# Optimization experiments

Measured on AMD Instinct MI355X. Metric: run time of the kernel, lower is better.

Reference implementation:

```python
import jax, jax.numpy as jnp
import numpy as np

N_QUBITS = 4
N_LAYERS = 2
_I2 = jnp.eye(2, dtype=jnp.complex64)
_X = jnp.array([[0.0, 1.0], [1.0, 0.0]], dtype=jnp.complex64)


def _apply_1q_batched(state, U, wire):
    # state: [B,2,2,2,2] complex, U: [B,2,2] (per-sample gate)
    s = jnp.moveaxis(state, 1 + wire, -1)
    s = jnp.einsum('bij,b...j->b...i', U, s)
    return jnp.moveaxis(s, -1, 1 + wire)


def _apply_1q(state, U, wire):
    # shared 2x2 gate on `wire`
    s = jnp.moveaxis(state, 1 + wire, -1)
    s = jnp.einsum('ij,...j->...i', U, s)
    return jnp.moveaxis(s, -1, 1 + wire)


def _apply_cnot(state, c, t):
    s = jnp.moveaxis(state, (1 + c, 1 + t), (-2, -1))  # [...,2(ctrl),2(tgt)]
    s = jnp.stack([s[..., 0, :], s[..., 1, ::-1]], axis=-2)  # flip target if ctrl=1
    return jnp.moveaxis(s, (-2, -1), (1 + c, 1 + t))


def _rot_matrix(phi, theta, omega):
    # qml.Rot = RZ(omega) @ RY(theta) @ RZ(phi)
    c, s = jnp.cos(theta / 2), jnp.sin(theta / 2)
    ep = jnp.exp(-0.5j * (phi + omega))  # e^{-i(phi+omega)/2}
    em = jnp.exp(-0.5j * (phi - omega))  # e^{-i(phi-omega)/2}
    return jnp.stack([
        jnp.stack([ep * c, -jnp.conj(em) * s]),
        jnp.stack([em * s, jnp.conj(ep) * c]),
    ]).astype(jnp.complex64)


def _circuit(angles, weights):
    # angles: [B, 4] real; weights: [2, 4, 3] real -> [B, 4] PauliZ expvals
    B = angles.shape[0]
    state = jnp.zeros((B,) + (2,) * N_QUBITS, jnp.complex64)
    state = state.at[(slice(None),) + (0,) * N_QUBITS].set(1.0)  # |0000>
    # AngleEmbedding (rotation='X'): RX(angle_w) on wire w, batched over samples
    for w in range(N_QUBITS):
        half = angles[:, w] / 2
        c, s = jnp.cos(half), jnp.sin(half)
        U = c[:, None, None] * _I2 - 1j * s[:, None, None] * _X  # [B,2,2]
        state = _apply_1q_batched(state, U, w)
    # StronglyEntanglingLayers: Rot on each wire, then ring of CNOTs with range r
    for l in range(N_LAYERS):
        for w in range(N_QUBITS):
            U = _rot_matrix(weights[l, w, 0], weights[l, w, 1], weights[l, w, 2])
            state = _apply_1q(state, U, w)
        r = (l % (N_QUBITS - 1)) + 1  # PennyLane default ranges
        for w in range(N_QUBITS):
            state = _apply_cnot(state, w, (w + r) % N_QUBITS)
    probs = state.real ** 2 + state.imag ** 2  # [B,2,2,2,2]
    z = []
    for w in range(N_QUBITS):
        other = tuple(a for a in range(1, N_QUBITS + 1) if a != 1 + w)
        p = probs.sum(other)  # [B,2]
        z.append(p[:, 0] - p[:, 1])
    return jnp.stack(z, axis=-1)  # [B,4]


def setup_inputs() -> dict:
    key = jax.random.key(0)
    ks = jax.random.split(key, 6)
    B, D_IN, D_OUT, NQ = 65536, 512, 512, N_QUBITS
    x = jax.random.normal(ks[0], (B, D_IN), jnp.float32)
    pre_W = jax.random.normal(ks[1], (NQ, D_IN), jnp.float32) / np.sqrt(D_IN)
    pre_b = jax.random.normal(ks[2], (NQ,), jnp.float32) * 0.05
    weights = jax.random.uniform(ks[3], (N_LAYERS, NQ, 3), jnp.float32) * (2 * np.pi)
    post_W = jax.random.normal(ks[4], (D_OUT, NQ), jnp.float32) / np.sqrt(NQ)
    post_b = jax.random.normal(ks[5], (D_OUT,), jnp.float32) * 0.05
    return {"x": x, "pre_W": pre_W, "pre_b": pre_b, "weights": weights,
            "post_W": post_W, "post_b": post_b}


def reference(x, pre_W, pre_b, weights, post_W, post_b):
    angles = jnp.tanh(x @ pre_W.T + pre_b) * jnp.pi  # [B,4]
    q = _circuit(angles, weights)                    # [B,4]
    return q @ post_W.T + post_b                     # [B,512]
```

## Files before the change

kernel.cpp:

```cpp
#include <hip/hip_runtime.h>
#include <math.h>

#define PI_F 3.14159265358979323846f


typedef float floatx4 __attribute__((ext_vector_type(4)));

static __device__ __forceinline__ void st_store4(float* p, floatx4 v)
{
    *reinterpret_cast<floatx4*>(p) = v;
}

static __device__ __forceinline__ float fast_tanh(float a)
{
    a = fminf(fmaxf(a, -15.f), 15.f);
    const float e = __expf(2.f * a);
    return (e - 1.f) / (e + 1.f);
}

template<int WIRE>
__device__ __forceinline__ void apply1q(float* sr, float* si,
    float u00r, float u00i, float u01r, float u01i,
    float u10r, float u10i, float u11r, float u11i)
{
    constexpr int st = 1 << (3 - WIRE);
#pragma unroll
    for (int i = 0; i < 16; ++i) {
        if (i & st) continue;
        const int j = i | st;
        const float r0 = sr[i], m0 = si[i], r1 = sr[j], m1 = si[j];
        sr[i] = u00r * r0 - u00i * m0 + u01r * r1 - u01i * m1;
        si[i] = u00r * m0 + u00i * r0 + u01r * m1 + u01i * r1;
        sr[j] = u10r * r0 - u10i * m0 + u11r * r1 - u11i * m1;
        si[j] = u10r * m0 + u10i * r0 + u11r * m1 + u11i * r1;
    }
}

template<int CW, int TW>
__device__ __forceinline__ void cnot(float* sr, float* si)
{
    constexpr int cb = 1 << (3 - CW), tb = 1 << (3 - TW);
#pragma unroll
    for (int i = 0; i < 16; ++i) {
        if ((i & cb) && !(i & tb)) {
            const int j = i | tb;
            float t;
            t = sr[i]; sr[i] = sr[j]; sr[j] = t;
            t = si[i]; si[i] = si[j]; si[j] = t;
        }
    }
}

#define APPLY_FAST(L, W) { \
    const float ph = wts[((L) * 4 + (W)) * 3 + 0]; \
    const float th = wts[((L) * 4 + (W)) * 3 + 1]; \
    const float om = wts[((L) * 4 + (W)) * 3 + 2]; \
    const float s_  = __sinf(0.5f * th),        c_  = __cosf(0.5f * th); \
    const float sp_ = __sinf(0.5f * (ph + om)), cp_ = __cosf(0.5f * (ph + om)); \
    const float sq_ = __sinf(0.5f * (ph - om)), cq_ = __cosf(0.5f * (ph - om)); \
    apply1q<W>(sr, si, cp_ * c_, -sp_ * c_, -cq_ * s_, -sq_ * s_, \
                       cq_ * s_, -sq_ * s_, cp_ * c_,  sp_ * c_); }

__global__ __launch_bounds__(256) void k_fused(
    const float* __restrict__ x,
    const float* __restrict__ preW,
    const float* __restrict__ preb,
    const float* __restrict__ wts,
    const float* __restrict__ postW,
    const float* __restrict__ postb,
    float* __restrict__ out, int B)
{
    const int lane  = threadIdx.x & 63;
    const int wid   = threadIdx.x >> 6;
    const int base  = blockIdx.x * 64;
    const int wbase = base + wid * 16;
    if (base >= B) return;

    __shared__ float4 angLds[64];

    float4 wA[4], wB[4];
#pragma unroll
    for (int w = 0; w < 4; ++w) {
        wA[w] = *reinterpret_cast<const float4*>(preW + w * 512 + lane * 4);
        wB[w] = *reinterpret_cast<const float4*>(preW + w * 512 + 256 + lane * 4);
    }
    const float4 pb = *reinterpret_cast<const float4*>(preb);

#pragma unroll
    for (int p = 0; p < 4; ++p) {
        const int b0 = wbase + p * 4;

        float4 xa[4], xb[4];
#pragma unroll
        for (int t = 0; t < 4; ++t) {
            const float* xr = x + (size_t)(b0 + t) * 512;
            xa[t] = *reinterpret_cast<const float4*>(xr + lane * 4);
            xb[t] = *reinterpret_cast<const float4*>(xr + 256 + lane * 4);
        }

        float acc[4][4];
#pragma unroll
        for (int t = 0; t < 4; ++t) {
#pragma unroll
            for (int w = 0; w < 4; ++w) {
                acc[t][w] = xa[t].x * wA[w].x + xa[t].y * wA[w].y + xa[t].z * wA[w].z + xa[t].w * wA[w].w
                          + xb[t].x * wB[w].x + xb[t].y * wB[w].y + xb[t].z * wB[w].z + xb[t].w * wB[w].w;
            }
        }

        float v[4];
#pragma unroll
        for (int t = 0; t < 4; ++t) {
            float a01 = (lane & 1) ? acc[t][1] : acc[t][0];
            float b01 = (lane & 1) ? acc[t][0] : acc[t][1];
            a01 += __shfl_xor(b01, 1, 64);
            float a23 = (lane & 1) ? acc[t][3] : acc[t][2];
            float b23 = (lane & 1) ? acc[t][2] : acc[t][3];
            a23 += __shfl_xor(b23, 1, 64);
            const float vv = (lane & 2) ? a23 : a01;
            const float uu = (lane & 2) ? a01 : a23;
            v[t] = vv + __shfl_xor(uu, 2, 64);
        }
        float c01 = (lane & 4) ? v[1] : v[0];
        float d01 = (lane & 4) ? v[0] : v[1];
        c01 += __shfl_xor(d01, 4, 64);
        float c23 = (lane & 4) ? v[3] : v[2];
        float d23 = (lane & 4) ? v[2] : v[3];
        c23 += __shfl_xor(d23, 4, 64);
        float m = (lane & 8) ? c23 : c01;
        float n = (lane & 8) ? c01 : c23;
        m += __shfl_xor(n, 8, 64);
        m += __shfl_xor(m, 16, 64);
        m += __shfl_xor(m, 32, 64);

        const float pb01 = (lane & 1) ? pb.y : pb.x;
        const float pb23 = (lane & 1) ? pb.w : pb.z;
        const float pbv  = (lane & 2) ? pb23 : pb01;
        const float angv = fast_tanh(m + pbv) * PI_F;

        if (lane < 16) {
            float* arow = reinterpret_cast<float*>(&angLds[wid * 16 + p * 4 + (lane >> 2)]);
            arow[lane & 3] = angv;
        }
    }

    __syncthreads();

    const int sid = lane >> 2;
    const float4 ang = angLds[wid * 16 + sid];

    const float s0 = __sinf(0.5f * ang.x), c0 = __cosf(0.5f * ang.x);
    const float s1 = __sinf(0.5f * ang.y), c1 = __cosf(0.5f * ang.y);
    const float s2 = __sinf(0.5f * ang.z), c2 = __cosf(0.5f * ang.z);
    const float s3 = __sinf(0.5f * ang.w), c3 = __cosf(0.5f * ang.w);

    float sr[16], si[16];
#pragma unroll
    for (int i = 0; i < 16; ++i) {
        const float r = ((i & 8) ? s0 : c0) * ((i & 4) ? s1 : c1)
                      * ((i & 2) ? s2 : c2) * ((i & 1) ? s3 : c3);
        const int mm = (((i >> 3) & 1) + ((i >> 2) & 1) + ((i >> 1) & 1) + (i & 1)) & 3;
        switch (mm) {
            case 0:  sr[i] = r;    si[i] = 0.f; break;
            case 1:  sr[i] = 0.f;  si[i] = -r;  break;
            case 2:  sr[i] = -r;   si[i] = 0.f; break;
            default: sr[i] = 0.f;  si[i] = r;   break;
        }
    }

    APPLY_FAST(0, 0); APPLY_FAST(0, 1); APPLY_FAST(0, 2); APPLY_FAST(0, 3);
    cnot<0, 1>(sr, si); cnot<1, 2>(sr, si); cnot<2, 3>(sr, si); cnot<3, 0>(sr, si);
    APPLY_FAST(1, 0); APPLY_FAST(1, 1); APPLY_FAST(1, 2); APPLY_FAST(1, 3);
    cnot<0, 2>(sr, si); cnot<1, 3>(sr, si); cnot<2, 0>(sr, si); cnot<3, 1>(sr, si);

    float z0 = 0.f, z1 = 0.f, z2 = 0.f, z3 = 0.f;
#pragma unroll
    for (int i = 0; i < 16; ++i) {
        const float p = sr[i] * sr[i] + si[i] * si[i];
        z0 += (i & 8) ? -p : p;
        z1 += (i & 4) ? -p : p;
        z2 += (i & 2) ? -p : p;
        z3 += (i & 1) ? -p : p;
    }

    const float4* pW4 = reinterpret_cast<const float4*>(postW);
    const float4* pb4 = reinterpret_cast<const float4*>(postb);
    const float4 p0 = pW4[4 * lane + 0], p1 = pW4[4 * lane + 1];
    const float4 p2 = pW4[4 * lane + 2], p3 = pW4[4 * lane + 3];
    const float4 p4 = pW4[4 * (64 + lane) + 0], p5 = pW4[4 * (64 + lane) + 1];
    const float4 p6 = pW4[4 * (64 + lane) + 2], p7 = pW4[4 * (64 + lane) + 3];
    const float4 bb0 = pb4[lane], bb1 = pb4[64 + lane];

#pragma unroll
    for (int s = 0; s < 16; ++s) {
        const float q0 = __shfl(z0, s * 4, 64);
        const float q1 = __shfl(z1, s * 4, 64);
        const float q2 = __shfl(z2, s * 4, 64);
        const float q3 = __shfl(z3, s * 4, 64);
        floatx4 o0, o1;
        o0.x = fmaf(q3, p0.w, fmaf(q2, p0.z, fmaf(q1, p0.y, fmaf(q0, p0.x, bb0.x))));
        o0.y = fmaf(q3, p1.w, fmaf(q2, p1.z, fmaf(q1, p1.y, fmaf(q0, p1.x, bb0.y))));
        o0.z = fmaf(q3, p2.w, fmaf(q2, p2.z, fmaf(q1, p2.y, fmaf(q0, p2.x, bb0.z))));
        o0.w = fmaf(q3, p3.w, fmaf(q2, p3.z, fmaf(q1, p3.y, fmaf(q0, p3.x, bb0.w))));
        o1.x = fmaf(q3, p4.w, fmaf(q2, p4.z, fmaf(q1, p4.y, fmaf(q0, p4.x, bb1.x))));
        o1.y = fmaf(q3, p5.w, fmaf(q2, p5.z, fmaf(q1, p5.y, fmaf(q0, p5.x, bb1.y))));
        o1.z = fmaf(q3, p6.w, fmaf(q2, p6.z, fmaf(q1, p6.y, fmaf(q0, p6.x, bb1.z))));
        o1.w = fmaf(q3, p7.w, fmaf(q2, p7.z, fmaf(q1, p7.y, fmaf(q0, p7.x, bb1.w))));
        float* orow = out + (size_t)(wbase + s) * 512;
        st_store4(orow + 4 * lane, o0);
        st_store4(orow + 256 + 4 * lane, o1);
    }
}

extern "C" void kernel_launch(void* const* d_in, const int* in_sizes, int n_in,
                              void* d_out, int out_size, void* d_ws, size_t ws_size,
                              hipStream_t stream)
{
    const float* x     = (const float*)d_in[0];
    const float* preW  = (const float*)d_in[1];
    const float* preb  = (const float*)d_in[2];
    const float* wts   = (const float*)d_in[3];
    const float* postW = (const float*)d_in[4];
    const float* postb = (const float*)d_in[5];
    float* out = (float*)d_out;
    const int B = in_sizes[0] / 512;

    k_fused<<<dim3((B + 63) / 64), dim3(256), 0, stream>>>(
        x, preW, preb, wts, postW, postb, out, B);
}
```

Baseline: 50.34 us.

## Distribute 16-amplitude state vector across 4 lanes with shuffle-based gates

Result: faster. 46.13 us (-8.4%).

```diff
diff --git a/kernel.cpp b/kernel.cpp
--- a/kernel.cpp
+++ b/kernel.cpp
@@ -18,48 +18,51 @@
     return (e - 1.f) / (e + 1.f);
 }
 
-template<int WIRE>
-__device__ __forceinline__ void apply1q(float* sr, float* si,
+template<int ST>
+__device__ __forceinline__ void rot_inlane(float* ar, float* ai,
     float u00r, float u00i, float u01r, float u01i,
     float u10r, float u10i, float u11r, float u11i)
 {
-    constexpr int st = 1 << (3 - WIRE);
-#pragma unroll
-    for (int i = 0; i < 16; ++i) {
-        if (i & st) continue;
-        const int j = i | st;
-        const float r0 = sr[i], m0 = si[i], r1 = sr[j], m1 = si[j];
-        sr[i] = u00r * r0 - u00i * m0 + u01r * r1 - u01i * m1;
-        si[i] = u00r * m0 + u00i * r0 + u01r * m1 + u01i * r1;
-        sr[j] = u10r * r0 - u10i * m0 + u11r * r1 - u11i * m1;
-        si[j] = u10r * m0 + u10i * r0 + u11r * m1 + u11i * r1;
-    }
-}
-
-template<int CW, int TW>
-__device__ __forceinline__ void cnot(float* sr, float* si)
-{
-    constexpr int cb = 1 << (3 - CW), tb = 1 << (3 - TW);
-#pragma unroll
-    for (int i = 0; i < 16; ++i) {
-        if ((i & cb) && !(i & tb)) {
-            const int j = i | tb;
-            float t;
-            t = sr[i]; sr[i] = sr[j]; sr[j] = t;
-            t = si[i]; si[i] = si[j]; si[j] = t;
-        }
-    }
-}
-
-#define APPLY_FAST(L, W) { \
-    const float ph = wts[((L) * 4 + (W)) * 3 + 0]; \
-    const float th = wts[((L) * 4 + (W)) * 3 + 1]; \
-    const float om = wts[((L) * 4 + (W)) * 3 + 2]; \
-    const float s_  = __sinf(0.5f * th),        c_  = __cosf(0.5f * th); \
-    const float sp_ = __sinf(0.5f * (ph + om)), cp_ = __cosf(0.5f * (ph + om)); \
-    const float sq_ = __sinf(0.5f * (ph - om)), cq_ = __cosf(0.5f * (ph - om)); \
-    apply1q<W>(sr, si, cp_ * c_, -sp_ * c_, -cq_ * s_, -sq_ * s_, \
-                       cq_ * s_, -sq_ * s_, cp_ * c_,  sp_ * c_); }
+#pragma unroll
+    for (int k = 0; k < 4; ++k) {
+        if (k & ST) continue;
+        const int j = k | ST;
+        const float Ar = ar[k], Ai = ai[k], Br = ar[j], Bi = ai[j];
+        ar[k] = u00r*Ar - u00i*Ai + u01r*Br - u01i*Bi;
+        ai[k] = u00r*Ai + u00i*Ar + u01r*Bi + u01i*Br;
+        ar[j] = u10r*Ar - u10i*Ai + u11r*Br - u11i*Bi;
+        ai[j] = u10r*Ai + u10i*Ar + u11r*Bi + u11i*Br;
+    }
+}
+
+template<int XM>
+__device__ __forceinline__ void rot_cross(float* ar, float* ai, bool ownB,
+    float u00r, float u00i, float u01r, float u01i,
+    float u10r, float u10i, float u11r, float u11i)
+{
+    const float cAr = ownB ? u11r : u00r;
+    const float cAi = ownB ? u11i : u00i;
+    const float cBr = ownB ? u10r : u01r;
+    const float cBi = ownB ? u10i : u01i;
+#pragma unroll
+    for (int k = 0; k < 4; ++k) {
+        const float pr = __shfl_xor(ar[k], XM, 64);
+        const float pi = __shfl_xor(ai[k], XM, 64);
+        const float vr = ar[k], vi = ai[k];
+        ar[k] = cAr*vr - cAi*vi + cBr*pr - cBi*pi;
+        ai[k] = cAr*vi + cAi*vr + cBr*pi + cBi*pr;
+    }
+}
+
+#define ROT_COEFFS(L, W) \
+    const float ph = wts[((L)*4+(W))*3+0]; \
+    const float th = wts[((L)*4+(W))*3+1]; \
+    const float om = wts[((L)*4+(W))*3+2]; \
+    const float s_  = __sinf(0.5f*th),        c_  = __cosf(0.5f*th); \
+    const float sp_ = __sinf(0.5f*(ph+om)),   cp_ = __cosf(0.5f*(ph+om)); \
+    const float sq_ = __sinf(0.5f*(ph-om)),   cq_ = __cosf(0.5f*(ph-om));
+
+#define U_ARGS cp_*c_, -sp_*c_, -cq_*s_, -sq_*s_, cq_*s_, -sq_*s_, cp_*c_, sp_*c_
 
 __global__ __launch_bounds__(256) void k_fused(
     const float* __restrict__ x,
@@ -146,7 +149,9 @@
 
     __syncthreads();
 
-    const int sid = lane >> 2;
+    const int  sid = lane >> 2;
+    const bool lb3 = (lane & 2) != 0;
+    const bool lb2 = (lane & 1) != 0;
     const float4 ang = angLds[wid * 16 + sid];
 
     const float s0 = __sinf(0.5f * ang.x), c0 = __cosf(0.5f * ang.x);
@@ -154,41 +159,97 @@
     const float s2 = __sinf(0.5f * ang.z), c2 = __cosf(0.5f * ang.z);
     const float s3 = __sinf(0.5f * ang.w), c3 = __cosf(0.5f * ang.w);
 
-    float sr[16], si[16];
-#pragma unroll
-    for (int i = 0; i < 16; ++i) {
-        const float r = ((i & 8) ? s0 : c0) * ((i & 4) ? s1 : c1)
-                      * ((i & 2) ? s2 : c2) * ((i & 1) ? s3 : c3);
-        const int mm = (((i >> 3) & 1) + ((i >> 2) & 1) + ((i >> 1) & 1) + (i & 1)) & 3;
-        switch (mm) {
-            case 0:  sr[i] = r;    si[i] = 0.f; break;
-            case 1:  sr[i] = 0.f;  si[i] = -r;  break;
-            case 2:  sr[i] = -r;   si[i] = 0.f; break;
-            default: sr[i] = 0.f;  si[i] = r;   break;
-        }
-    }
-
-    APPLY_FAST(0, 0); APPLY_FAST(0, 1); APPLY_FAST(0, 2); APPLY_FAST(0, 3);
-    cnot<0, 1>(sr, si); cnot<1, 2>(sr, si); cnot<2, 3>(sr, si); cnot<3, 0>(sr, si);
-    APPLY_FAST(1, 0); APPLY_FAST(1, 1); APPLY_FAST(1, 2); APPLY_FAST(1, 3);
-    cnot<0, 2>(sr, si); cnot<1, 3>(sr, si); cnot<2, 0>(sr, si); cnot<3, 1>(sr, si);
-
-    float z0 = 0.f, z1 = 0.f, z2 = 0.f, z3 = 0.f;
-#pragma unroll
-    for (int i = 0; i < 16; ++i) {
-        const float p = sr[i] * sr[i] + si[i] * si[i];
-        z0 += (i & 8) ? -p : p;
-        z1 += (i & 4) ? -p : p;
-        z2 += (i & 2) ? -p : p;
-        z3 += (i & 1) ? -p : p;
-    }
+    const float mhi = (lb3 ? s0 : c0) * (lb2 ? s1 : c1);
+    const float hr  = lb3 ? (lb2 ? -mhi : 0.f) : (lb2 ? 0.f : mhi);
+    const float hi  = (lb3 != lb2) ? -mhi : 0.f;
+    const float low0 = c2 * c3, low1 = c2 * s3, low2 = s2 * c3, low3 = s2 * s3;
+
+    float ar[4], ai[4];
+    ar[0] =  hr * low0;  ai[0] =  hi * low0;
+    ar[1] =  hi * low1;  ai[1] = -hr * low1;
+    ar[2] =  hi * low2;  ai[2] = -hr * low2;
+    ar[3] = -hr * low3;  ai[3] = -hi * low3;
+
+    { ROT_COEFFS(0, 0); rot_cross<2>(ar, ai, lb3, U_ARGS); }
+    { ROT_COEFFS(0, 1); rot_cross<1>(ar, ai, lb2, U_ARGS); }
+    { ROT_COEFFS(0, 2); rot_inlane<2>(ar, ai, U_ARGS); }
+    { ROT_COEFFS(0, 3); rot_inlane<1>(ar, ai, U_ARGS); }
+
+    {
+#pragma unroll
+        for (int k = 0; k < 4; ++k) {
+            const float tr = __shfl_xor(ar[k], 1, 64);
+            const float ti = __shfl_xor(ai[k], 1, 64);
+            ar[k] = lb3 ? tr : ar[k];
+            ai[k] = lb3 ? ti : ai[k];
+        }
+    }
+    {
+        const float t0r = ar[0], t0i = ai[0], t1r = ar[1], t1i = ai[1];
+        ar[0] = lb2 ? ar[2] : ar[0];  ai[0] = lb2 ? ai[2] : ai[0];
+        ar[1] = lb2 ? ar[3] : ar[1];  ai[1] = lb2 ? ai[3] : ai[1];
+        ar[2] = lb2 ? t0r   : ar[2];  ai[2] = lb2 ? t0i   : ai[2];
+        ar[3] = lb2 ? t1r   : ar[3];  ai[3] = lb2 ? t1i   : ai[3];
+    }
+    {
+        float t;
+        t = ar[2]; ar[2] = ar[3]; ar[3] = t;
+        t = ai[2]; ai[2] = ai[3]; ai[3] = t;
+    }
+    {
+        ar[1] = __shfl_xor(ar[1], 2, 64);  ai[1] = __shfl_xor(ai[1], 2, 64);
+        ar[3] = __shfl_xor(ar[3], 2, 64);  ai[3] = __shfl_xor(ai[3], 2, 64);
+    }
+
+    { ROT_COEFFS(1, 0); rot_cross<2>(ar, ai, lb3, U_ARGS); }
+    { ROT_COEFFS(1, 1); rot_cross<1>(ar, ai, lb2, U_ARGS); }
+    { ROT_COEFFS(1, 2); rot_inlane<2>(ar, ai, U_ARGS); }
+    { ROT_COEFFS(1, 3); rot_inlane<1>(ar, ai, U_ARGS); }
+
+    {
+        const float t0r = ar[0], t0i = ai[0], t1r = ar[1], t1i = ai[1];
+        ar[0] = lb3 ? ar[2] : ar[0];  ai[0] = lb3 ? ai[2] : ai[0];
+        ar[1] = lb3 ? ar[3] : ar[1];  ai[1] = lb3 ? ai[3] : ai[1];
+        ar[2] = lb3 ? t0r   : ar[2];  ai[2] = lb3 ? t0i   : ai[2];
+        ar[3] = lb3 ? t1r   : ar[3];  ai[3] = lb3 ? t1i   : ai[3];
+    }
+    {
+        const float t0r = ar[0], t0i = ai[0], t2r = ar[2], t2i = ai[2];
+        ar[0] = lb2 ? ar[1] : ar[0];  ai[0] = lb2 ? ai[1] : ai[0];
+        ar[1] = lb2 ? t0r   : ar[1];  ai[1] = lb2 ? t0i   : ai[1];
+        ar[2] = lb2 ? ar[3] : ar[2];  ai[2] = lb2 ? ai[3] : ai[2];
+        ar[3] = lb2 ? t2r   : ar[3];  ai[3] = lb2 ? t2i   : ai[3];
+    }
+    {
+        ar[2] = __shfl_xor(ar[2], 2, 64);  ai[2] = __shfl_xor(ai[2], 2, 64);
+        ar[3] = __shfl_xor(ar[3], 2, 64);  ai[3] = __shfl_xor(ai[3], 2, 64);
+    }
+    {
+        ar[1] = __shfl_xor(ar[1], 1, 64);  ai[1] = __shfl_xor(ai[1], 1, 64);
+        ar[3] = __shfl_xor(ar[3], 1, 64);  ai[3] = __shfl_xor(ai[3], 1, 64);
+    }
+
+    const float p0 = ar[0]*ar[0] + ai[0]*ai[0];
+    const float p1 = ar[1]*ar[1] + ai[1]*ai[1];
+    const float p2 = ar[2]*ar[2] + ai[2]*ai[2];
+    const float p3 = ar[3]*ar[3] + ai[3]*ai[3];
+    const float s01 = p0 + p1, s23 = p2 + p3;
+    const float sum = s01 + s23;
+    float z0 = lb3 ? -sum : sum;
+    float z1 = lb2 ? -sum : sum;
+    float z2 = s01 - s23;
+    float z3 = (p0 - p1) + (p2 - p3);
+    z0 += __shfl_xor(z0, 1, 64);  z0 += __shfl_xor(z0, 2, 64);
+    z1 += __shfl_xor(z1, 1, 64);  z1 += __shfl_xor(z1, 2, 64);
+    z2 += __shfl_xor(z2, 1, 64);  z2 += __shfl_xor(z2, 2, 64);
+    z3 += __shfl_xor(z3, 1, 64);  z3 += __shfl_xor(z3, 2, 64);
 
     const float4* pW4 = reinterpret_cast<const float4*>(postW);
     const float4* pb4 = reinterpret_cast<const float4*>(postb);
-    const float4 p0 = pW4[4 * lane + 0], p1 = pW4[4 * lane + 1];
-    const float4 p2 = pW4[4 * lane + 2], p3 = pW4[4 * lane + 3];
-    const float4 p4 = pW4[4 * (64 + lane) + 0], p5 = pW4[4 * (64 + lane) + 1];
-    const float4 p6 = pW4[4 * (64 + lane) + 2], p7 = pW4[4 * (64 + lane) + 3];
+    const float4 q0w = pW4[4 * lane + 0], q1w = pW4[4 * lane + 1];
+    const float4 q2w = pW4[4 * lane + 2], q3w = pW4[4 * lane + 3];
+    const float4 q4w = pW4[4 * (64 + lane) + 0], q5w = pW4[4 * (64 + lane) + 1];
+    const float4 q6w = pW4[4 * (64 + lane) + 2], q7w = pW4[4 * (64 + lane) + 3];
     const float4 bb0 = pb4[lane], bb1 = pb4[64 + lane];
 
 #pragma unroll
@@ -198,14 +259,14 @@
         const float q2 = __shfl(z2, s * 4, 64);
         const float q3 = __shfl(z3, s * 4, 64);
         floatx4 o0, o1;
-        o0.x = fmaf(q3, p0.w, fmaf(q2, p0.z, fmaf(q1, p0.y, fmaf(q0, p0.x, bb0.x))));
-        o0.y = fmaf(q3, p1.w, fmaf(q2, p1.z, fmaf(q1, p1.y, fmaf(q0, p1.x, bb0.y))));
-        o0.z = fmaf(q3, p2.w, fmaf(q2, p2.z, fmaf(q1, p2.y, fmaf(q0, p2.x, bb0.z))));
-        o0.w = fmaf(q3, p3.w, fmaf(q2, p3.z, fmaf(q1, p3.y, fmaf(q0, p3.x, bb0.w))));
-        o1.x = fmaf(q3, p4.w, fmaf(q2, p4.z, fmaf(q1, p4.y, fmaf(q0, p4.x, bb1.x))));
-        o1.y = fmaf(q3, p5.w, fmaf(q2, p5.z, fmaf(q1, p5.y, fmaf(q0, p5.x, bb1.y))));
-        o1.z = fmaf(q3, p6.w, fmaf(q2, p6.z, fmaf(q1, p6.y, fmaf(q0, p6.x, bb1.z))));
-        o1.w = fmaf(q3, p7.w, fmaf(q2, p7.z, fmaf(q1, p7.y, fmaf(q0, p7.x, bb1.w))));
+        o0.x = fmaf(q3, q0w.w, fmaf(q2, q0w.z, fmaf(q1, q0w.y, fmaf(q0, q0w.x, bb0.x))));
+        o0.y = fmaf(q3, q1w.w, fmaf(q2, q1w.z, fmaf(q1, q1w.y, fmaf(q0, q1w.x, bb0.y))));
+        o0.z = fmaf(q3, q2w.w, fmaf(q2, q2w.z, fmaf(q1, q2w.y, fmaf(q0, q2w.x, bb0.z))));
+        o0.w = fmaf(q3, q3w.w, fmaf(q2, q3w.z, fmaf(q1, q3w.y, fmaf(q0, q3w.x, bb0.w))));
+        o1.x = fmaf(q3, q4w.w, fmaf(q2, q4w.z, fmaf(q1, q4w.y, fmaf(q0, q4w.x, bb1.x))));
+        o1.y = fmaf(q3, q5w.w, fmaf(q2, q5w.z, fmaf(q1, q5w.y, fmaf(q0, q5w.x, bb1.y))));
+        o1.z = fmaf(q3, q6w.w, fmaf(q2, q6w.z, fmaf(q1, q6w.y, fmaf(q0, q6w.x, bb1.z))));
+        o1.w = fmaf(q3, q7w.w, fmaf(q2, q7w.z, fmaf(q1, q7w.y, fmaf(q0, q7w.x, bb1.w))));
         float* orow = out + (size_t)(wbase + s) * 512;
         st_store4(orow + 4 * lane, o0);
         st_store4(orow + 256 + 4 * lane, o1);
```
